# Optimization experiments

Hardware: AMD Instinct MI355X
Metric: run time of the kernel (lower is better)

## Reference

```python
import jax, jax.numpy as jnp
import numpy as np

B, C, W, H = 8, 256, 64, 64
CQ = C // 8  # f/g projection dim


def setup_inputs() -> dict:
    key = jax.random.key(0)
    ks = jax.random.split(key, 8)
    x = jax.random.normal(ks[0], (B, C, W, H), dtype=jnp.float32)
    y = jax.random.normal(ks[1], (B, C, W, H), dtype=jnp.float32)
    # 1x1 conv weights stored as [out, in] matrices (xavier-uniform-like scale)
    def xavier(k, o, i):
        lim = float(np.sqrt(6.0 / (o + i)))
        return jax.random.uniform(k, (o, i), dtype=jnp.float32, minval=-lim, maxval=lim)
    Wf = xavier(ks[2], CQ, C); bf = jnp.zeros((CQ,), jnp.float32)
    Wg = xavier(ks[3], CQ, C); bg = jnp.zeros((CQ,), jnp.float32)
    Wh = xavier(ks[4], C, C);  bh = jnp.zeros((C,), jnp.float32)
    gamma = jnp.zeros((1,), jnp.float32)
    return {"x": x, "y": y, "Wf": Wf, "bf": bf, "Wg": Wg, "bg": bg,
            "Wh": Wh, "bh": bh, "gamma": gamma}


def reference(x, y, Wf, bf, Wg, bg, Wh, bh, gamma):
    b, c, w, h = x.shape
    n = w * h
    xf = x.reshape(b, c, n)  # [B,C,N]
    yf = y.reshape(b, c, n)
    f = jnp.einsum('dc,bcn->bdn', Wf, xf) + bf[None, :, None]  # [B,CQ,N]
    g = jnp.einsum('dc,bcn->bdn', Wg, yf) + bg[None, :, None]  # [B,CQ,N]
    hh = jnp.einsum('dc,bcn->bdn', Wh, xf) + bh[None, :, None]  # [B,C,N]
    # attention[b,i,j] = sum_d f[b,d,i] * g[b,d,j]; softmax over j (no 1/sqrt(d) scaling)
    attn = jax.nn.softmax(jnp.einsum('bdi,bdj->bij', f, g), axis=-1)  # [B,N,N]
    sa = jnp.einsum('bcn,bin->bci', hh, attn.transpose(0, 2, 1))  # h @ attn: [B,C,N]
    sa = jnp.einsum('bcj,bij->bci', hh, attn)  # equivalent, clean: sum_j h[:, :, j]*attn[:, i, j]
    out = gamma[0] * sa.reshape(b, c, w, h) + x
    return out
```

## Files before the change

### kernel.cpp

```cpp
#include <hip/hip_runtime.h>
#include <math.h>

#define BB      8
#define C_DIM   256
#define NN      4096
#define CQ_DIM  32
#define LOG2E   1.44269504088896f

typedef __bf16 bf16_t;
typedef bf16_t bf16x4 __attribute__((ext_vector_type(4)));
typedef bf16_t bf16x8 __attribute__((ext_vector_type(8)));
typedef float  f32x16 __attribute__((ext_vector_type(16)));

#if defined(__has_builtin)
#if __has_builtin(__builtin_amdgcn_exp2f)
#define EXP2F(x) __builtin_amdgcn_exp2f(x)
#else
#define EXP2F(x) exp2f(x)
#endif
#else
#define EXP2F(x) exp2f(x)
#endif

#define MFMA32(a, b, c) __builtin_amdgcn_mfma_f32_32x32x16_bf16((a), (b), (c), 0, 0, 0)

__device__ __forceinline__ void gload_lds16(const bf16_t* g, bf16_t* l)
{
    __builtin_amdgcn_global_load_lds(
        (const __attribute__((address_space(1))) void*)g,
        (__attribute__((address_space(3))) void*)l, 16, 0, 0);
}

__global__ __launch_bounds__(256) void cast_weights(
    const float* __restrict__ Wh, const float* __restrict__ Wf,
    const float* __restrict__ Wg, bf16_t* __restrict__ Whp,
    bf16_t* __restrict__ Wfp, bf16_t* __restrict__ Wgp)
{
    const int id = blockIdx.x * 256 + threadIdx.x;
    if (id < 65536) {
        const int e = id & 7, lane = (id >> 3) & 63;
        const int s = (id >> 9) & 15, m = id >> 13;
        const int l31 = lane & 31, half = lane >> 5;
        Whp[id] = (bf16_t)Wh[(m * 32 + l31) * 256 + s * 16 + half * 8 + e];
    } else if (id < 73728) {
        const int q = id - 65536;
        const int e = q & 7, lane = (q >> 3) & 63, s = q >> 9;
        const int l31 = lane & 31, half = lane >> 5;
        Wfp[q] = (bf16_t)Wf[l31 * 256 + s * 16 + half * 8 + e];
    } else if (id < 81920) {
        const int q = id - 73728;
        const int e = q & 7, lane = (q >> 3) & 63, s = q >> 9;
        const int l31 = lane & 31, half = lane >> 5;
        Wgp[q] = (bf16_t)Wg[l31 * 256 + s * 16 + half * 8 + e];
    }
}

__global__ __launch_bounds__(256) void prep_fused(
    const float* __restrict__ x, const float* __restrict__ y,
    const bf16_t* __restrict__ Whp, const bf16_t* __restrict__ Wfp,
    const bf16_t* __restrict__ Wgp,
    const float* __restrict__ bh, const float* __restrict__ bfv,
    const float* __restrict__ bg,
    bf16_t* __restrict__ Qw, bf16_t* __restrict__ Kw, bf16_t* __restrict__ Vw)
{
    const int id = blockIdx.x;
    const int b  = id & 7;
    const int n0 = (id >> 3) * 64;

    __shared__ __align__(16) bf16_t Xb[64 * 256];
    __shared__ __align__(16) bf16_t Yb[64 * 256];

    const int t = threadIdx.x;
    const int w = t >> 6, lane = t & 63, l31 = lane & 31, half = lane >> 5;

    const int crow0 = w * 2 + (lane >> 5);
    const int nA = (lane & 31) * 2, nB = nA + 1;
    const size_t off0 = ((size_t)b * C_DIM + crow0) * NN + n0 + nA;

    float2 xv[32];
#pragma unroll
    for (int i = 0; i < 32; ++i)
        xv[i] = *(const float2*)(x + off0 + (size_t)(i * 8) * NN);

#pragma unroll
    for (int i = 0; i < 32; ++i) {
        Xb[nA * 256 + ((i ^ (nA & 15)) << 3) + crow0] = (bf16_t)xv[i].x;
        Xb[nB * 256 + ((i ^ (nB & 15)) << 3) + crow0] = (bf16_t)xv[i].y;
    }

    float2 yv[32];
#pragma unroll
    for (int i = 0; i < 32; ++i)
        yv[i] = *(const float2*)(y + off0 + (size_t)(i * 8) * NN);
    asm volatile("" ::: "memory");

    __syncthreads();

    auto bfrag = [&](const bf16_t* buf, int nloc, int s) -> bf16x8 {
        return *(const bf16x8*)&buf[nloc * 256 +
                                    (((s * 2 + half) ^ (nloc & 15)) << 3)];
    };

    if (w < 2) {
        const int nloc = w * 32 + l31;
        const bf16_t* Wp = Wfp + lane * 8;
        f32x16 acc = {};
        for (int s = 0; s < 16; ++s) {
            const bf16x8 af = *(const bf16x8*)(Wp + s * 512);
            acc = MFMA32(af, bfrag(Xb, nloc, s), acc);
        }
        bf16_t* dst = Qw + ((size_t)b * NN + n0 + nloc) * CQ_DIM;
#pragma unroll
        for (int rq = 0; rq < 4; ++rq) {
            const int d0 = 8 * rq + 4 * half;
            bf16x4 v4;
#pragma unroll
            for (int ri = 0; ri < 4; ++ri)
                v4[ri] = (bf16_t)(acc[4 * rq + ri] + bfv[d0 + ri]);
            *(bf16x4*)(dst + d0) = v4;
        }
    }

#pragma unroll
    for (int mi = 0; mi < 2; ++mi) {
        const int m = 2 * w + mi;
        const bf16_t* Ap = Whp + (size_t)m * 8192 + lane * 8;
        f32x16 a0 = {}, a1 = {};
        for (int s = 0; s < 16; ++s) {
            const bf16x8 af = *(const bf16x8*)(Ap + s * 512);
            a0 = MFMA32(af, bfrag(Xb, l31, s), a0);
            a1 = MFMA32(af, bfrag(Xb, 32 + l31, s), a1);
        }
#pragma unroll
        for (int r = 0; r < 16; ++r) {
            const int co = m * 32 + (r & 3) + 8 * (r >> 2) + 4 * half;
            const float bb = bh[co];
            bf16_t* vp = Vw + ((size_t)b * C_DIM + co) * NN + n0 + l31;
            vp[0]  = (bf16_t)(a0[r] + bb);
            vp[32] = (bf16_t)(a1[r] + bb);
        }
    }

#pragma unroll
    for (int i = 0; i < 32; ++i) {
        Yb[nA * 256 + ((i ^ (nA & 15)) << 3) + crow0] = (bf16_t)yv[i].x;
        Yb[nB * 256 + ((i ^ (nB & 15)) << 3) + crow0] = (bf16_t)yv[i].y;
    }
    __syncthreads();

    if (w < 2) {
        const int nloc = w * 32 + l31;
        const bf16_t* Wp = Wgp + lane * 8;
        f32x16 acc = {};
        for (int s = 0; s < 16; ++s) {
            const bf16x8 af = *(const bf16x8*)(Wp + s * 512);
            acc = MFMA32(af, bfrag(Yb, nloc, s), acc);
        }
        bf16_t* dst = Kw + ((size_t)b * NN + n0 + nloc) * CQ_DIM;
#pragma unroll
        for (int rq = 0; rq < 4; ++rq) {
            const int d0 = 8 * rq + 4 * half;
            bf16x4 v4;
#pragma unroll
            for (int ri = 0; ri < 4; ++ri)
                v4[ri] = (bf16_t)(acc[4 * rq + ri] + bg[d0 + ri]);
            *(bf16x4*)(dst + d0) = v4;
        }
    }
}

__global__ __launch_bounds__(512, 2) void attn_fused(
    const bf16_t* __restrict__ Q, const bf16_t* __restrict__ K,
    const bf16_t* __restrict__ V, const float* __restrict__ x,
    const float* __restrict__ gamma, float* __restrict__ out)
{
    const int id = blockIdx.x;
    const int b  = id & 7;
    const int i0 = (id >> 3) * 64;
    const int t  = threadIdx.x;
    const int w = t >> 6, lane = t & 63, l31 = lane & 31, half = lane >> 5;
    const int qg = w >> 2;
    const int jg = w & 3;
    const int cbx = ((jg & 1) << 2) | (jg & 2);

    __shared__ __align__(16) bf16_t Vlds[2][256 * 128];
    __shared__ float lpart[4 * 64];
    __shared__ float linv_s[64];

    const int r8h = 8 * half;

    const bf16_t* Qp = Q + ((size_t)(b * NN + i0 + qg * 32 + l31)) * CQ_DIM + r8h;
    const bf16x8 qf0 = *(const bf16x8*)Qp;
    const bf16x8 qf1 = *(const bf16x8*)(Qp + 16);

    const int pj = (l31 & 19) | ((l31 & 4) << 1) | ((l31 & 8) >> 1);
    const bf16_t* Kcur = K + ((size_t)b * NN + jg * 32 + pj) * CQ_DIM + r8h;

    const int sa = lane & 15, sb = lane >> 4;
    const bf16_t* Vrow0 = V + ((size_t)b * C_DIM + w * 32 + sb) * NN;
    int joff[8];
#pragma unroll
    for (int i = 0; i < 8; ++i)
        joff[i] = 8 * (sa ^ ((i * 4 + sb) & 15));

    const int vsw  = l31 & 15;
    const int vrow = l31 * 128;
    const int p0 = (((jg * 4) + half) ^ vsw) << 3;
    const int p1 = (((jg * 4) + 2 + half) ^ vsw) << 3;

    float lacc = 0.f;
    f32x16 O[8] = {{}, {}, {}, {}, {}, {}, {}, {}};
    bf16x8 frag[2];

    bf16_t* vcur = &Vlds[0][0];
    bf16_t* vnxt = &Vlds[1][0];

    auto do_stage = [&](int j0e, bf16_t* vb) {
        bf16_t* d = vb + w * 4096;
#pragma unroll
        for (int i = 0; i < 8; ++i)
            gload_lds16(Vrow0 + (size_t)(i * 4) * NN + j0e + joff[i],
                        d + i * 512);
    };

    auto do_exp = [&](const f32x16& sv) {
        bf16x8 q0, q1;
#pragma unroll
        for (int r = 0; r < 8; ++r) {
            const float pv = EXP2F(sv[r] * LOG2E);
            lacc += pv; q0[r] = (bf16_t)pv;
        }
#pragma unroll
        for (int r = 8; r < 16; ++r) {
            const float pv = EXP2F(sv[r] * LOG2E);
            lacc += pv; q1[r - 8] = (bf16_t)pv;
        }
        frag[0] = q0;
        frag[1] = q1;
    };

    auto do_PV = [&](const bf16_t* vb) {
#pragma unroll
        for (int i = 0; i < 8; ++i) {
            const int rb = ((i ^ cbx) << 12) + vrow;
            const bf16x8 v0 = *(const bf16x8*)&vb[rb + p0];
            const bf16x8 v1 = *(const bf16x8*)&vb[rb + p1];
            O[i] = MFMA32(frag[0], v0, O[i]);
            O[i] = MFMA32(frag[1], v1, O[i]);
        }
    };

    {
        const bf16x8 k0 = *(const bf16x8*)Kcur;
        const bf16x8 k1 = *(const bf16x8*)(Kcur + 16);
        Kcur += 128 * CQ_DIM;
        do_stage(0, vcur);
        f32x16 sv = {};
        sv = MFMA32(k0, qf0, sv);
        sv = MFMA32(k1, qf1, sv);
        do_exp(sv);
    }
    __syncthreads();

    for (int tt = 0; tt < 31; ++tt) {
        const bf16x8 k0 = *(const bf16x8*)Kcur;
        const bf16x8 k1 = *(const bf16x8*)(Kcur + 16);
        Kcur += 128 * CQ_DIM;
        do_stage((tt + 1) * 128, vnxt);
        __builtin_amdgcn_s_setprio(1);
        do_PV(vcur);
        f32x16 sv = {};
        sv = MFMA32(k0, qf0, sv);
        sv = MFMA32(k1, qf1, sv);
        __builtin_amdgcn_s_setprio(0);
        do_exp(sv);
        __syncthreads();
        bf16_t* tmp = vcur; vcur = vnxt; vnxt = tmp;
    }
    __builtin_amdgcn_s_setprio(1);
    do_PV(vcur);
    __builtin_amdgcn_s_setprio(0);

    lacc += __shfl_xor(lacc, 32, 64);
    if (half == 0) lpart[jg * 64 + qg * 32 + l31] = lacc;
    __syncthreads();
    if (t < 64)
        linv_s[t] = 1.0f / (lpart[t] + lpart[64 + t] + lpart[128 + t] + lpart[192 + t]);

    float* red = (float*)&Vlds[0][0];
    const int qsw = l31 & 7;
    const int myA = w * 4096;

    {
        float* s = red + myA;
#pragma unroll
        for (int k = 0; k < 4; ++k)
#pragma unroll
            for (int r4 = 0; r4 < 4; ++r4) {
                const int quad = 2 * r4 + half;
                float4 v4 = { O[4 + k][4 * r4 + 0], O[4 + k][4 * r4 + 1],
                              O[4 + k][4 * r4 + 2], O[4 + k][4 * r4 + 3] };
                *(float4*)&s[k * 1024 + l31 * 32 + ((quad ^ qsw) << 2)] = v4;
            }
    }
    __syncthreads();
    {
        const float* s = red + (w ^ 1) * 4096;
#pragma unroll
        for (int k = 0; k < 4; ++k)
#pragma unroll
            for (int r4 = 0; r4 < 4; ++r4) {
                const int quad = 2 * r4 + half;
                const float4 v4 = *(const float4*)&s[k * 1024 + l31 * 32 + ((quad ^ qsw) << 2)];
                O[k][4 * r4 + 0] += v4.x;
                O[k][4 * r4 + 1] += v4.y;
                O[k][4 * r4 + 2] += v4.z;
                O[k][4 * r4 + 3] += v4.w;
            }
    }
    __syncthreads();
    {
        float* s = red + myA;
#pragma unroll
        for (int k = 0; k < 2; ++k)
#pragma unroll
            for (int r4 = 0; r4 < 4; ++r4) {
                const int quad = 2 * r4 + half;
                float4 v4 = { O[2 + k][4 * r4 + 0], O[2 + k][4 * r4 + 1],
                              O[2 + k][4 * r4 + 2], O[2 + k][4 * r4 + 3] };
                *(float4*)&s[k * 1024 + l31 * 32 + ((quad ^ qsw) << 2)] = v4;
            }
    }
    __syncthreads();
    {
        const float* s = red + (w ^ 2) * 4096;
#pragma unroll
        for (int k = 0; k < 2; ++k)
#pragma unroll
            for (int r4 = 0; r4 < 4; ++r4) {
                const int quad = 2 * r4 + half;
                const float4 v4 = *(const float4*)&s[k * 1024 + l31 * 32 + ((quad ^ qsw) << 2)];
                O[k][4 * r4 + 0] += v4.x;
                O[k][4 * r4 + 1] += v4.y;
                O[k][4 * r4 + 2] += v4.z;
                O[k][4 * r4 + 3] += v4.w;
            }
    }

    const float g = gamma[0];
#pragma unroll
    for (int k = 0; k < 2; ++k) {
        const int ch = (k ^ cbx) * 32 + l31;
        const size_t base = ((size_t)b * C_DIM + ch) * NN + i0 + qg * 32 + 4 * half;
#pragma unroll
        for (int r4 = 0; r4 < 4; ++r4) {
            const size_t idx = base + 8 * r4;
            const int rb = qg * 32 + 8 * r4 + 4 * half;
            const float4 xv = *(const float4*)(x + idx);
            float4 o;
            o.x = fmaf(g, O[k][4 * r4 + 0] * linv_s[rb + 0], xv.x);
            o.y = fmaf(g, O[k][4 * r4 + 1] * linv_s[rb + 1], xv.y);
            o.z = fmaf(g, O[k][4 * r4 + 2] * linv_s[rb + 2], xv.z);
            o.w = fmaf(g, O[k][4 * r4 + 3] * linv_s[rb + 3], xv.w);
            *(float4*)(out + idx) = o;
        }
    }
}

extern "C" void kernel_launch(void* const* d_in, const int* in_sizes, int n_in,
                              void* d_out, int out_size, void* d_ws, size_t ws_size,
                              hipStream_t stream)
{
    const float* x     = (const float*)d_in[0];
    const float* y     = (const float*)d_in[1];
    const float* Wf    = (const float*)d_in[2];
    const float* bf    = (const float*)d_in[3];
    const float* Wg    = (const float*)d_in[4];
    const float* bg    = (const float*)d_in[5];
    const float* Wh    = (const float*)d_in[6];
    const float* bh    = (const float*)d_in[7];
    const float* gamma = (const float*)d_in[8];
    float* out = (float*)d_out;

    bf16_t* bufA = (bf16_t*)d_ws;
    bf16_t* Qw   = bufA + (size_t)BB * NN * C_DIM;
    bf16_t* Kw   = Qw + (size_t)BB * NN * CQ_DIM;
    bf16_t* Whp  = Kw + (size_t)BB * NN * CQ_DIM;
    bf16_t* Wfp  = Whp + C_DIM * C_DIM;
    bf16_t* Wgp  = Wfp + CQ_DIM * C_DIM;

    cast_weights<<<320, 256, 0, stream>>>(Wh, Wf, Wg, Whp, Wfp, Wgp);
    prep_fused<<<512, 256, 0, stream>>>(x, y, Whp, Wfp, Wgp,
                                        bh, bf, bg, Qw, Kw, bufA);
    attn_fused<<<BB * (NN / 64), 512, 0, stream>>>(Qw, Kw, bufA, x, gamma, out);
}
```

Baseline: 227.6 us.

## Single-buffer V tiles and split prep kernel to raise occupancy

Splits the fused x/y projection kernel into two kernels with half the shared memory each and higher occupancy hints. In the attention kernel, replaces the double-buffered V staging with a single buffer synchronized twice per iteration. It also shrinks the cross-wave O reduction into three smaller passes so it fits the halved LDS, and requests four blocks per CU. This trades load/compute overlap and register budget (risking spills of the 128-float accumulator) for more resident waves.

```diff
diff --git a/kernel.cpp b/kernel.cpp
--- a/kernel.cpp
+++ b/kernel.cpp
@@ -55,20 +55,17 @@
     }
 }
 
-__global__ __launch_bounds__(256) void prep_fused(
-    const float* __restrict__ x, const float* __restrict__ y,
+__global__ __launch_bounds__(256, 4) void prep_x(
+    const float* __restrict__ x,
     const bf16_t* __restrict__ Whp, const bf16_t* __restrict__ Wfp,
-    const bf16_t* __restrict__ Wgp,
     const float* __restrict__ bh, const float* __restrict__ bfv,
-    const float* __restrict__ bg,
-    bf16_t* __restrict__ Qw, bf16_t* __restrict__ Kw, bf16_t* __restrict__ Vw)
+    bf16_t* __restrict__ Qw, bf16_t* __restrict__ Vw)
 {
     const int id = blockIdx.x;
     const int b  = id & 7;
     const int n0 = (id >> 3) * 64;
 
     __shared__ __align__(16) bf16_t Xb[64 * 256];
-    __shared__ __align__(16) bf16_t Yb[64 * 256];
 
     const int t = threadIdx.x;
     const int w = t >> 6, lane = t & 63, l31 = lane & 31, half = lane >> 5;
@@ -81,24 +78,16 @@
 #pragma unroll
     for (int i = 0; i < 32; ++i)
         xv[i] = *(const float2*)(x + off0 + (size_t)(i * 8) * NN);
-
 #pragma unroll
     for (int i = 0; i < 32; ++i) {
         Xb[nA * 256 + ((i ^ (nA & 15)) << 3) + crow0] = (bf16_t)xv[i].x;
         Xb[nB * 256 + ((i ^ (nB & 15)) << 3) + crow0] = (bf16_t)xv[i].y;
     }
-
-    float2 yv[32];
-#pragma unroll
-    for (int i = 0; i < 32; ++i)
-        yv[i] = *(const float2*)(y + off0 + (size_t)(i * 8) * NN);
-    asm volatile("" ::: "memory");
-
     __syncthreads();
 
-    auto bfrag = [&](const bf16_t* buf, int nloc, int s) -> bf16x8 {
-        return *(const bf16x8*)&buf[nloc * 256 +
-                                    (((s * 2 + half) ^ (nloc & 15)) << 3)];
+    auto bfrag = [&](int nloc, int s) -> bf16x8 {
+        return *(const bf16x8*)&Xb[nloc * 256 +
+                                   (((s * 2 + half) ^ (nloc & 15)) << 3)];
     };
 
     if (w < 2) {
@@ -107,7 +96,7 @@
         f32x16 acc = {};
         for (int s = 0; s < 16; ++s) {
             const bf16x8 af = *(const bf16x8*)(Wp + s * 512);
-            acc = MFMA32(af, bfrag(Xb, nloc, s), acc);
+            acc = MFMA32(af, bfrag(nloc, s), acc);
         }
         bf16_t* dst = Qw + ((size_t)b * NN + n0 + nloc) * CQ_DIM;
 #pragma unroll
@@ -128,8 +117,8 @@
         f32x16 a0 = {}, a1 = {};
         for (int s = 0; s < 16; ++s) {
             const bf16x8 af = *(const bf16x8*)(Ap + s * 512);
-            a0 = MFMA32(af, bfrag(Xb, l31, s), a0);
-            a1 = MFMA32(af, bfrag(Xb, 32 + l31, s), a1);
+            a0 = MFMA32(af, bfrag(l31, s), a0);
+            a1 = MFMA32(af, bfrag(32 + l31, s), a1);
         }
 #pragma unroll
         for (int r = 0; r < 16; ++r) {
@@ -140,7 +129,30 @@
             vp[32] = (bf16_t)(a1[r] + bb);
         }
     }
-
+}
+
+__global__ __launch_bounds__(256, 4) void prep_y(
+    const float* __restrict__ y,
+    const bf16_t* __restrict__ Wgp, const float* __restrict__ bg,
+    bf16_t* __restrict__ Kw)
+{
+    const int id = blockIdx.x;
+    const int b  = id & 7;
+    const int n0 = (id >> 3) * 64;
+
+    __shared__ __align__(16) bf16_t Yb[64 * 256];
+
+    const int t = threadIdx.x;
+    const int w = t >> 6, lane = t & 63, l31 = lane & 31, half = lane >> 5;
+
+    const int crow0 = w * 2 + (lane >> 5);
+    const int nA = (lane & 31) * 2, nB = nA + 1;
+    const size_t off0 = ((size_t)b * C_DIM + crow0) * NN + n0 + nA;
+
+    float2 yv[32];
+#pragma unroll
+    for (int i = 0; i < 32; ++i)
+        yv[i] = *(const float2*)(y + off0 + (size_t)(i * 8) * NN);
 #pragma unroll
     for (int i = 0; i < 32; ++i) {
         Yb[nA * 256 + ((i ^ (nA & 15)) << 3) + crow0] = (bf16_t)yv[i].x;
@@ -154,7 +166,9 @@
         f32x16 acc = {};
         for (int s = 0; s < 16; ++s) {
             const bf16x8 af = *(const bf16x8*)(Wp + s * 512);
-            acc = MFMA32(af, bfrag(Yb, nloc, s), acc);
+            const bf16x8 bf = *(const bf16x8*)&Yb[nloc * 256 +
+                                (((s * 2 + half) ^ (nloc & 15)) << 3)];
+            acc = MFMA32(af, bf, acc);
         }
         bf16_t* dst = Kw + ((size_t)b * NN + n0 + nloc) * CQ_DIM;
 #pragma unroll
@@ -169,7 +183,7 @@
     }
 }
 
-__global__ __launch_bounds__(512, 2) void attn_fused(
+__global__ __launch_bounds__(512, 4) void attn_fused(
     const bf16_t* __restrict__ Q, const bf16_t* __restrict__ K,
     const bf16_t* __restrict__ V, const float* __restrict__ x,
     const float* __restrict__ gamma, float* __restrict__ out)
@@ -183,7 +197,7 @@
     const int jg = w & 3;
     const int cbx = ((jg & 1) << 2) | (jg & 2);
 
-    __shared__ __align__(16) bf16_t Vlds[2][256 * 128];
+    __shared__ __align__(16) bf16_t Vlds[256 * 128];
     __shared__ float lpart[4 * 64];
     __shared__ float linv_s[64];
 
@@ -212,11 +226,8 @@
     f32x16 O[8] = {{}, {}, {}, {}, {}, {}, {}, {}};
     bf16x8 frag[2];
 
-    bf16_t* vcur = &Vlds[0][0];
-    bf16_t* vnxt = &Vlds[1][0];
-
-    auto do_stage = [&](int j0e, bf16_t* vb) {
-        bf16_t* d = vb + w * 4096;
+    auto do_stage = [&](int j0e) {
+        bf16_t* d = Vlds + w * 4096;
 #pragma unroll
         for (int i = 0; i < 8; ++i)
             gload_lds16(Vrow0 + (size_t)(i * 4) * NN + j0e + joff[i],
@@ -239,12 +250,12 @@
         frag[1] = q1;
     };
 
-    auto do_PV = [&](const bf16_t* vb) {
+    auto do_PV = [&]() {
 #pragma unroll
         for (int i = 0; i < 8; ++i) {
             const int rb = ((i ^ cbx) << 12) + vrow;
-            const bf16x8 v0 = *(const bf16x8*)&vb[rb + p0];
-            const bf16x8 v1 = *(const bf16x8*)&vb[rb + p1];
+            const bf16x8 v0 = *(const bf16x8*)&Vlds[rb + p0];
+            const bf16x8 v1 = *(const bf16x8*)&Vlds[rb + p1];
             O[i] = MFMA32(frag[0], v0, O[i]);
             O[i] = MFMA32(frag[1], v1, O[i]);
         }
@@ -254,32 +265,28 @@
         const bf16x8 k0 = *(const bf16x8*)Kcur;
         const bf16x8 k1 = *(const bf16x8*)(Kcur + 16);
         Kcur += 128 * CQ_DIM;
-        do_stage(0, vcur);
         f32x16 sv = {};
         sv = MFMA32(k0, qf0, sv);
         sv = MFMA32(k1, qf1, sv);
         do_exp(sv);
     }
-    __syncthreads();
 
     for (int tt = 0; tt < 31; ++tt) {
+        do_stage(tt * 128);
         const bf16x8 k0 = *(const bf16x8*)Kcur;
         const bf16x8 k1 = *(const bf16x8*)(Kcur + 16);
         Kcur += 128 * CQ_DIM;
-        do_stage((tt + 1) * 128, vnxt);
-        __builtin_amdgcn_s_setprio(1);
-        do_PV(vcur);
+        __syncthreads();
+        do_PV();
         f32x16 sv = {};
         sv = MFMA32(k0, qf0, sv);
         sv = MFMA32(k1, qf1, sv);
-        __builtin_amdgcn_s_setprio(0);
         do_exp(sv);
         __syncthreads();
-        bf16_t* tmp = vcur; vcur = vnxt; vnxt = tmp;
-    }
-    __builtin_amdgcn_s_setprio(1);
-    do_PV(vcur);
-    __builtin_amdgcn_s_setprio(0);
+    }
+    do_stage(31 * 128);
+    __syncthreads();
+    do_PV();
 
     lacc += __shfl_xor(lacc, 32, 64);
     if (half == 0) lpart[jg * 64 + qg * 32 + l31] = lacc;
@@ -287,64 +294,43 @@
     if (t < 64)
         linv_s[t] = 1.0f / (lpart[t] + lpart[64 + t] + lpart[128 + t] + lpart[192 + t]);
 
-    float* red = (float*)&Vlds[0][0];
+    float* red = (float*)Vlds;
     const int qsw = l31 & 7;
-    const int myA = w * 4096;
-
-    {
-        float* s = red + myA;
-#pragma unroll
-        for (int k = 0; k < 4; ++k)
-#pragma unroll
-            for (int r4 = 0; r4 < 4; ++r4) {
-                const int quad = 2 * r4 + half;
-                float4 v4 = { O[4 + k][4 * r4 + 0], O[4 + k][4 * r4 + 1],
-                              O[4 + k][4 * r4 + 2], O[4 + k][4 * r4 + 3] };
-                *(float4*)&s[k * 1024 + l31 * 32 + ((quad ^ qsw) << 2)] = v4;
-            }
-    }
-    __syncthreads();
-    {
-        const float* s = red + (w ^ 1) * 4096;
-#pragma unroll
-        for (int k = 0; k < 4; ++k)
-#pragma unroll
-            for (int r4 = 0; r4 < 4; ++r4) {
-                const int quad = 2 * r4 + half;
-                const float4 v4 = *(const float4*)&s[k * 1024 + l31 * 32 + ((quad ^ qsw) << 2)];
-                O[k][4 * r4 + 0] += v4.x;
-                O[k][4 * r4 + 1] += v4.y;
-                O[k][4 * r4 + 2] += v4.z;
-                O[k][4 * r4 + 3] += v4.w;
-            }
-    }
-    __syncthreads();
-    {
-        float* s = red + myA;
-#pragma unroll
-        for (int k = 0; k < 2; ++k)
-#pragma unroll
-            for (int r4 = 0; r4 < 4; ++r4) {
-                const int quad = 2 * r4 + half;
-                float4 v4 = { O[2 + k][4 * r4 + 0], O[2 + k][4 * r4 + 1],
-                              O[2 + k][4 * r4 + 2], O[2 + k][4 * r4 + 3] };
-                *(float4*)&s[k * 1024 + l31 * 32 + ((quad ^ qsw) << 2)] = v4;
-            }
-    }
-    __syncthreads();
-    {
-        const float* s = red + (w ^ 2) * 4096;
-#pragma unroll
-        for (int k = 0; k < 2; ++k)
-#pragma unroll
-            for (int r4 = 0; r4 < 4; ++r4) {
-                const int quad = 2 * r4 + half;
-                const float4 v4 = *(const float4*)&s[k * 1024 + l31 * 32 + ((quad ^ qsw) << 2)];
-                O[k][4 * r4 + 0] += v4.x;
-                O[k][4 * r4 + 1] += v4.y;
-                O[k][4 * r4 + 2] += v4.z;
-                O[k][4 * r4 + 3] += v4.w;
-            }
+    const int myA = w * 2048;
+
+#pragma unroll
+    for (int pass = 0; pass < 3; ++pass) {
+        const int src = (pass == 0) ? 4 : (pass == 1) ? 6 : 2;
+        const int dst = (pass == 1) ? 2 : 0;
+        const int dw  = (pass == 2) ? 2 : 1;
+        {
+            float* s = red + myA;
+#pragma unroll
+            for (int k = 0; k < 2; ++k)
+#pragma unroll
+                for (int r4 = 0; r4 < 4; ++r4) {
+                    const int quad = 2 * r4 + half;
+                    float4 v4 = { O[src + k][4 * r4 + 0], O[src + k][4 * r4 + 1],
+                                  O[src + k][4 * r4 + 2], O[src + k][4 * r4 + 3] };
+                    *(float4*)&s[k * 1024 + l31 * 32 + ((quad ^ qsw) << 2)] = v4;
+                }
+        }
+        __syncthreads();
+        {
+            const float* s = red + (w ^ dw) * 2048;
+#pragma unroll
+            for (int k = 0; k < 2; ++k)
+#pragma unroll
+                for (int r4 = 0; r4 < 4; ++r4) {
+                    const int quad = 2 * r4 + half;
+                    const float4 v4 = *(const float4*)&s[k * 1024 + l31 * 32 + ((quad ^ qsw) << 2)];
+                    O[dst + k][4 * r4 + 0] += v4.x;
+                    O[dst + k][4 * r4 + 1] += v4.y;
+                    O[dst + k][4 * r4 + 2] += v4.z;
+                    O[dst + k][4 * r4 + 3] += v4.w;
+                }
+        }
+        __syncthreads();
     }
 
     const float g = gamma[0];
@@ -390,7 +376,7 @@
     bf16_t* Wgp  = Wfp + CQ_DIM * C_DIM;
 
     cast_weights<<<320, 256, 0, stream>>>(Wh, Wf, Wg, Whp, Wfp, Wgp);
-    prep_fused<<<512, 256, 0, stream>>>(x, y, Whp, Wfp, Wgp,
-                                        bh, bf, bg, Qw, Kw, bufA);
+    prep_x<<<512, 256, 0, stream>>>(x, Whp, Wfp, bh, bf, Qw, bufA);
+    prep_y<<<512, 256, 0, stream>>>(y, Wgp, bg, Kw);
     attn_fused<<<BB * (NN / 64), 512, 0, stream>>>(Qw, Kw, bufA, x, gamma, out);
 }
```

Result: slower. 755.7 us (+232.1%).

## Double query tile per block to halve V staging and cut reduction stages

Applied to the files above, without the earlier changes.

Each attention block now handles 128 query rows instead of 64. Warps are split into 4 query groups by 2 key groups, and each warp computes two 32-key score tiles per step. Every staged V tile in LDS is therefore shared across twice as many queries, which halves global V traffic, and the cross-warp output reduction drops from two stages to one. In exchange the grid is half as large, each warp carries more registers, and the s_setprio hints were removed.

```diff
diff --git a/kernel.cpp b/kernel.cpp
--- a/kernel.cpp
+++ b/kernel.cpp
@@ -81,7 +81,6 @@
 #pragma unroll
     for (int i = 0; i < 32; ++i)
         xv[i] = *(const float2*)(x + off0 + (size_t)(i * 8) * NN);
-
 #pragma unroll
     for (int i = 0; i < 32; ++i) {
         Xb[nA * 256 + ((i ^ (nA & 15)) << 3) + crow0] = (bf16_t)xv[i].x;
@@ -176,16 +175,16 @@
 {
     const int id = blockIdx.x;
     const int b  = id & 7;
-    const int i0 = (id >> 3) * 64;
+    const int i0 = (id >> 3) * 128;
     const int t  = threadIdx.x;
     const int w = t >> 6, lane = t & 63, l31 = lane & 31, half = lane >> 5;
-    const int qg = w >> 2;
-    const int jg = w & 3;
-    const int cbx = ((jg & 1) << 2) | (jg & 2);
+    const int qg = w >> 1;
+    const int jg = w & 1;
+    const int cbx = jg << 2;
 
     __shared__ __align__(16) bf16_t Vlds[2][256 * 128];
-    __shared__ float lpart[4 * 64];
-    __shared__ float linv_s[64];
+    __shared__ float lpart[2 * 128];
+    __shared__ float linv_s[128];
 
     const int r8h = 8 * half;
 
@@ -194,7 +193,7 @@
     const bf16x8 qf1 = *(const bf16x8*)(Qp + 16);
 
     const int pj = (l31 & 19) | ((l31 & 4) << 1) | ((l31 & 8) >> 1);
-    const bf16_t* Kcur = K + ((size_t)b * NN + jg * 32 + pj) * CQ_DIM + r8h;
+    const bf16_t* Kcur = K + ((size_t)b * NN + jg * 64 + pj) * CQ_DIM + r8h;
 
     const int sa = lane & 15, sb = lane >> 4;
     const bf16_t* Vrow0 = V + ((size_t)b * C_DIM + w * 32 + sb) * NN;
@@ -205,15 +204,16 @@
 
     const int vsw  = l31 & 15;
     const int vrow = l31 * 128;
-    const int p0 = (((jg * 4) + half) ^ vsw) << 3;
-    const int p1 = (((jg * 4) + 2 + half) ^ vsw) << 3;
+    int po[4];
+#pragma unroll
+    for (int jj = 0; jj < 2; ++jj)
+#pragma unroll
+        for (int f = 0; f < 2; ++f)
+            po[jj * 2 + f] = (((jg * 8 + jj * 4 + f * 2 + half)) ^ vsw) << 3;
 
     float lacc = 0.f;
     f32x16 O[8] = {{}, {}, {}, {}, {}, {}, {}, {}};
-    bf16x8 frag[2];
-
-    bf16_t* vcur = &Vlds[0][0];
-    bf16_t* vnxt = &Vlds[1][0];
+    bf16x8 frag[4];
 
     auto do_stage = [&](int j0e, bf16_t* vb) {
         bf16_t* d = vb + w * 4096;
@@ -223,74 +223,78 @@
                         d + i * 512);
     };
 
-    auto do_exp = [&](const f32x16& sv) {
-        bf16x8 q0, q1;
-#pragma unroll
-        for (int r = 0; r < 8; ++r) {
-            const float pv = EXP2F(sv[r] * LOG2E);
-            lacc += pv; q0[r] = (bf16_t)pv;
-        }
-#pragma unroll
-        for (int r = 8; r < 16; ++r) {
-            const float pv = EXP2F(sv[r] * LOG2E);
-            lacc += pv; q1[r - 8] = (bf16_t)pv;
-        }
-        frag[0] = q0;
-        frag[1] = q1;
+    auto do_S = [&](const bf16x8* kf) {
+#pragma unroll
+        for (int jj = 0; jj < 2; ++jj) {
+            f32x16 sv = {};
+            sv = MFMA32(kf[jj * 2],     qf0, sv);
+            sv = MFMA32(kf[jj * 2 + 1], qf1, sv);
+            bf16x8 q0, q1;
+#pragma unroll
+            for (int r = 0; r < 8; ++r) {
+                const float pv = EXP2F(sv[r] * LOG2E);
+                lacc += pv; q0[r] = (bf16_t)pv;
+            }
+#pragma unroll
+            for (int r = 8; r < 16; ++r) {
+                const float pv = EXP2F(sv[r] * LOG2E);
+                lacc += pv; q1[r - 8] = (bf16_t)pv;
+            }
+            frag[jj * 2]     = q0;
+            frag[jj * 2 + 1] = q1;
+        }
     };
 
     auto do_PV = [&](const bf16_t* vb) {
 #pragma unroll
         for (int i = 0; i < 8; ++i) {
             const int rb = ((i ^ cbx) << 12) + vrow;
-            const bf16x8 v0 = *(const bf16x8*)&vb[rb + p0];
-            const bf16x8 v1 = *(const bf16x8*)&vb[rb + p1];
-            O[i] = MFMA32(frag[0], v0, O[i]);
-            O[i] = MFMA32(frag[1], v1, O[i]);
+#pragma unroll
+            for (int fi = 0; fi < 4; ++fi) {
+                const bf16x8 v0 = *(const bf16x8*)&vb[rb + po[fi]];
+                O[i] = MFMA32(frag[fi], v0, O[i]);
+            }
         }
     };
 
     {
-        const bf16x8 k0 = *(const bf16x8*)Kcur;
-        const bf16x8 k1 = *(const bf16x8*)(Kcur + 16);
+        bf16x8 kf[4];
+        kf[0] = *(const bf16x8*)Kcur;
+        kf[1] = *(const bf16x8*)(Kcur + 16);
+        kf[2] = *(const bf16x8*)(Kcur + 1024);
+        kf[3] = *(const bf16x8*)(Kcur + 1024 + 16);
         Kcur += 128 * CQ_DIM;
-        do_stage(0, vcur);
-        f32x16 sv = {};
-        sv = MFMA32(k0, qf0, sv);
-        sv = MFMA32(k1, qf1, sv);
-        do_exp(sv);
-    }
-    __syncthreads();
-
+        do_stage(0, &Vlds[0][0]);
+        do_S(kf);
+    }
+    __syncthreads();
+
+    bf16_t* vcur = &Vlds[0][0];
+    bf16_t* vnxt = &Vlds[1][0];
     for (int tt = 0; tt < 31; ++tt) {
-        const bf16x8 k0 = *(const bf16x8*)Kcur;
-        const bf16x8 k1 = *(const bf16x8*)(Kcur + 16);
+        bf16x8 kf[4];
+        kf[0] = *(const bf16x8*)Kcur;
+        kf[1] = *(const bf16x8*)(Kcur + 16);
+        kf[2] = *(const bf16x8*)(Kcur + 1024);
+        kf[3] = *(const bf16x8*)(Kcur + 1024 + 16);
         Kcur += 128 * CQ_DIM;
         do_stage((tt + 1) * 128, vnxt);
-        __builtin_amdgcn_s_setprio(1);
         do_PV(vcur);
-        f32x16 sv = {};
-        sv = MFMA32(k0, qf0, sv);
-        sv = MFMA32(k1, qf1, sv);
-        __builtin_amdgcn_s_setprio(0);
-        do_exp(sv);
+        do_S(kf);
         __syncthreads();
         bf16_t* tmp = vcur; vcur = vnxt; vnxt = tmp;
     }
-    __builtin_amdgcn_s_setprio(1);
     do_PV(vcur);
-    __builtin_amdgcn_s_setprio(0);
 
     lacc += __shfl_xor(lacc, 32, 64);
-    if (half == 0) lpart[jg * 64 + qg * 32 + l31] = lacc;
-    __syncthreads();
-    if (t < 64)
-        linv_s[t] = 1.0f / (lpart[t] + lpart[64 + t] + lpart[128 + t] + lpart[192 + t]);
+    if (half == 0) lpart[jg * 128 + qg * 32 + l31] = lacc;
+    __syncthreads();
+    if (t < 128)
+        linv_s[t] = 1.0f / (lpart[t] + lpart[128 + t]);
 
     float* red = (float*)&Vlds[0][0];
     const int qsw = l31 & 7;
     const int myA = w * 4096;
-
     {
         float* s = red + myA;
 #pragma unroll
@@ -318,38 +322,10 @@
                 O[k][4 * r4 + 3] += v4.w;
             }
     }
-    __syncthreads();
-    {
-        float* s = red + myA;
-#pragma unroll
-        for (int k = 0; k < 2; ++k)
-#pragma unroll
-            for (int r4 = 0; r4 < 4; ++r4) {
-                const int quad = 2 * r4 + half;
-                float4 v4 = { O[2 + k][4 * r4 + 0], O[2 + k][4 * r4 + 1],
-                              O[2 + k][4 * r4 + 2], O[2 + k][4 * r4 + 3] };
-                *(float4*)&s[k * 1024 + l31 * 32 + ((quad ^ qsw) << 2)] = v4;
-            }
-    }
-    __syncthreads();
-    {
-        const float* s = red + (w ^ 2) * 4096;
-#pragma unroll
-        for (int k = 0; k < 2; ++k)
-#pragma unroll
-            for (int r4 = 0; r4 < 4; ++r4) {
-                const int quad = 2 * r4 + half;
-                const float4 v4 = *(const float4*)&s[k * 1024 + l31 * 32 + ((quad ^ qsw) << 2)];
-                O[k][4 * r4 + 0] += v4.x;
-                O[k][4 * r4 + 1] += v4.y;
-                O[k][4 * r4 + 2] += v4.z;
-                O[k][4 * r4 + 3] += v4.w;
-            }
-    }
 
     const float g = gamma[0];
 #pragma unroll
-    for (int k = 0; k < 2; ++k) {
+    for (int k = 0; k < 4; ++k) {
         const int ch = (k ^ cbx) * 32 + l31;
         const size_t base = ((size_t)b * C_DIM + ch) * NN + i0 + qg * 32 + 4 * half;
 #pragma unroll
@@ -392,5 +368,5 @@
     cast_weights<<<320, 256, 0, stream>>>(Wh, Wf, Wg, Whp, Wfp, Wgp);
     prep_fused<<<512, 256, 0, stream>>>(x, y, Whp, Wfp, Wgp,
                                         bh, bf, bg, Qw, Kw, bufA);
-    attn_fused<<<BB * (NN / 64), 512, 0, stream>>>(Qw, Kw, bufA, x, gamma, out);
-}
+    attn_fused<<<BB * (NN / 128), 512, 0, stream>>>(Qw, Kw, bufA, x, gamma, out);
+}
```

Result: faster. 213.0 us (-6.4%).
